# Optimization experiments

Hardware: AMD Instinct MI355X
Metric: run time of the kernel (lower is better)

## Reference

```python
import jax, jax.numpy as jnp
import numpy as np

K = 2  # top-k experts per token


def setup_inputs() -> dict:
    key = jax.random.key(0)
    k1, k2 = jax.random.split(key)
    B, T, D, E = 4, 4096, 4096, 64
    x = jax.random.normal(k1, (B, T, D), dtype=jnp.float32)
    W = jax.random.normal(k2, (E, D), dtype=jnp.float32) * (1.0 / np.sqrt(D))
    return {"x": x, "W": W}


def reference(x, W):
    # router_logits: [B, T, E]  (nn.Linear with no bias: x @ W.T)
    router_logits = jnp.einsum('btd,ed->bte', x, W)
    # top-k over expert dim, then softmax over the k selected logits
    topk_logits, topk_idx = jax.lax.top_k(router_logits, K)  # [B,T,K]
    topk_weight = jax.nn.softmax(topk_logits, axis=-1)       # [B,T,K]
    return (topk_idx, topk_weight, router_logits)
```

## Files before the change

### kernel.cpp

```cpp
#include <hip/hip_runtime.h>
#include <math.h>

#define NTOK 16384
#define DDIM 4096
#define NEXP 64
#define TAU  2e-4f
#define WS_LO 262144
#define NCW  16

typedef short bf16x8 __attribute__((ext_vector_type(8)));
typedef float f32x4  __attribute__((ext_vector_type(4)));

__device__ __forceinline__ unsigned short bf16_rne(float f) {
  unsigned u = __float_as_uint(f);
  u += 0x7fffu + ((u >> 16) & 1u);
  return (unsigned short)(u >> 16);
}

__device__ __forceinline__ void split4(float4 v, uint2& hi, uint2& lo) {
  unsigned h0 = bf16_rne(v.x), h1 = bf16_rne(v.y), h2 = bf16_rne(v.z), h3 = bf16_rne(v.w);
  float r0 = v.x - __uint_as_float(h0 << 16);
  float r1 = v.y - __uint_as_float(h1 << 16);
  float r2 = v.z - __uint_as_float(h2 << 16);
  float r3 = v.w - __uint_as_float(h3 << 16);
  unsigned l0 = bf16_rne(r0), l1 = bf16_rne(r1), l2 = bf16_rne(r2), l3 = bf16_rne(r3);
  hi = make_uint2(h0 | (h1 << 16), h2 | (h3 << 16));
  lo = make_uint2(l0 | (l1 << 16), l2 | (l3 << 16));
}

__device__ __forceinline__ void split4v(f32x4 v, uint2& hi, uint2& lo) {
  unsigned h0 = bf16_rne(v[0]), h1 = bf16_rne(v[1]), h2 = bf16_rne(v[2]), h3 = bf16_rne(v[3]);
  float r0 = v[0] - __uint_as_float(h0 << 16);
  float r1 = v[1] - __uint_as_float(h1 << 16);
  float r2 = v[2] - __uint_as_float(h2 << 16);
  float r3 = v[3] - __uint_as_float(h3 << 16);
  unsigned l0 = bf16_rne(r0), l1 = bf16_rne(r1), l2 = bf16_rne(r2), l3 = bf16_rne(r3);
  hi = make_uint2(h0 | (h1 << 16), h2 | (h3 << 16));
  lo = make_uint2(l0 | (l1 << 16), l2 | (l3 << 16));
}

__device__ __forceinline__ bf16x8 mk8(uint2 a, uint2 b) {
  union { uint4 u; bf16x8 v; } t;
  t.u = make_uint4(a.x, a.y, b.x, b.y);
  return t.v;
}

__device__ __forceinline__ void gld_lds16(const float* g, char* l) {
  __builtin_amdgcn_global_load_lds((const __attribute__((address_space(1))) void*)g,
                                   (__attribute__((address_space(3))) void*)l,
                                   16, 0, 0);
}

__device__ __forceinline__ bool better(float va, int ia, float vb, int ib) {
  return (va > vb) || (va == vb && ia < ib);
}
__device__ __forceinline__ bool betterd(double va, int ia, double vb, int ib) {
  return (va > vb) || (va == vb && ia < ib);
}
#define CE(va, ia, vb, ib) { if (better(vb, ib, va, ia)) { float _tv = va; va = vb; vb = _tv; int _ti = ia; ia = ib; ib = _ti; } }

__global__ __launch_bounds__(256)
void presplit_w(const float* __restrict__ w, short* __restrict__ ws) {
  const int tid = blockIdx.x * 256 + threadIdx.x;
  const int e = tid >> 9;
  const int o = tid & 511;
  const int c = o >> 2, q = o & 3;
  const int l = (e & 15) + 16 * q;
  const int g = e >> 4;
  const float* src = w + (size_t)e * DDIM + o * 8;
  float4 v0 = *(const float4*)src;
  float4 v1 = *(const float4*)(src + 4);
  uint2 h0, s0, h1, s1;
  split4(v0, h0, s0);
  split4(v1, h1, s1);
  const int off = c * 2048 + g * 512 + l * 8;
  *(uint4*)(ws + off)         = make_uint4(h0.x, h0.y, h1.x, h1.y);
  *(uint4*)(ws + WS_LO + off) = make_uint4(s0.x, s0.y, s1.x, s1.y);
}

__device__ __noinline__ void fixup_token(const float* __restrict__ x,
                                         const float* __restrict__ wgt,
                                         float* __restrict__ out_idx,
                                         float* __restrict__ out_wt,
                                         int tok, unsigned pk, int l) {
  const int e0 = pk & 255, e1 = (pk >> 8) & 255, e2 = (pk >> 16) & 255, e3 = (pk >> 24) & 255;
  const float* xr = x   + (size_t)tok * DDIM + l * 64;
  const float* w0 = wgt + (size_t)e0 * DDIM + l * 64;
  const float* w1 = wgt + (size_t)e1 * DDIM + l * 64;
  const float* w2 = wgt + (size_t)e2 * DDIM + l * 64;
  const float* w3 = wgt + (size_t)e3 * DDIM + l * 64;
  double s0 = 0.0, s1 = 0.0, s2 = 0.0, s3 = 0.0;
#pragma unroll 4
  for (int j = 0; j < 64; j += 4) {
    float4 xv = *(const float4*)(xr + j);
    float4 av = *(const float4*)(w0 + j);
    s0 = fma((double)xv.x, (double)av.x, s0); s0 = fma((double)xv.y, (double)av.y, s0);
    s0 = fma((double)xv.z, (double)av.z, s0); s0 = fma((double)xv.w, (double)av.w, s0);
    av = *(const float4*)(w1 + j);
    s1 = fma((double)xv.x, (double)av.x, s1); s1 = fma((double)xv.y, (double)av.y, s1);
    s1 = fma((double)xv.z, (double)av.z, s1); s1 = fma((double)xv.w, (double)av.w, s1);
    av = *(const float4*)(w2 + j);
    s2 = fma((double)xv.x, (double)av.x, s2); s2 = fma((double)xv.y, (double)av.y, s2);
    s2 = fma((double)xv.z, (double)av.z, s2); s2 = fma((double)xv.w, (double)av.w, s2);
    av = *(const float4*)(w3 + j);
    s3 = fma((double)xv.x, (double)av.x, s3); s3 = fma((double)xv.y, (double)av.y, s3);
    s3 = fma((double)xv.z, (double)av.z, s3); s3 = fma((double)xv.w, (double)av.w, s3);
  }
#pragma unroll
  for (int m = 1; m < 64; m <<= 1) {
    s0 += __shfl_xor(s0, m);
    s1 += __shfl_xor(s1, m);
    s2 += __shfl_xor(s2, m);
    s3 += __shfl_xor(s3, m);
  }
  if (l == 0) {
    double v0 = s0, v1 = s1, v2 = s2, v3 = s3;
    int i0 = e0, i1 = e1, i2 = e2, i3 = e3;
    if (betterd(v1, i1, v0, i0)) { double tv = v0; v0 = v1; v1 = tv; int ti = i0; i0 = i1; i1 = ti; }
    if (betterd(v3, i3, v2, i2)) { double tv = v2; v2 = v3; v3 = tv; int ti = i2; i2 = i3; i3 = ti; }
    if (betterd(v2, i2, v0, i0)) { double tv = v0; v0 = v2; v2 = tv; int ti = i0; i0 = i2; i2 = ti; }
    if (betterd(v3, i3, v1, i1)) { double tv = v1; v1 = v3; v3 = tv; int ti = i1; i1 = i3; i3 = ti; }
    if (betterd(v2, i2, v1, i1)) { double tv = v1; v1 = v2; v2 = tv; int ti = i1; i1 = i2; i2 = ti; }
    double ex = exp(v1 - v0);
    double den = 1.0 + ex;
    out_idx[tok * 2 + 0] = (float)i0;
    out_idx[tok * 2 + 1] = (float)i1;
    out_wt[tok * 2 + 0]  = (float)(1.0 / den);
    out_wt[tok * 2 + 1]  = (float)(ex / den);
  }
}

__global__ __launch_bounds__(512, 3)
void router_main(const float* __restrict__ x, const float* __restrict__ wgt,
                 const short* __restrict__ ws, float* __restrict__ out) {
  __shared__ __align__(16) char ldsbuf[65536];

  const int u = threadIdx.x;
  const int l = u & 63;
  const int wid = u >> 6;
  const int tokBase = blockIdx.x * 32;

  char* ring = ldsbuf + wid * 8192;
  const unsigned ldsbase =
      (unsigned)(size_t)(__attribute__((address_space(3))) char*)&ldsbuf[0];
  const unsigned rbase = ldsbase + wid * 8192 + l * 16;

  const int P = (blockIdx.x * 5) & 15;
#define PHYS(T) (((T) + P) & 15)

  const float* xA0 = x + (size_t)(tokBase +  0 + (l & 15)) * DDIM + wid * 512 + (l >> 4) * 8;
  const float* xB0 = xA0 + 4;
  const float* xA1 = x + (size_t)(tokBase + 16 + (l & 15)) * DDIM + wid * 512 + (l >> 4) * 8;
  const float* xB1 = xA1 + 4;

  const short* wch = ws + wid * 32768 + l * 8;

  f32x4 acc[2][4];
#pragma unroll
  for (int t2 = 0; t2 < 2; ++t2)
#pragma unroll
    for (int g = 0; g < 4; ++g) acc[t2][g] = (f32x4){0.f, 0.f, 0.f, 0.f};

  bf16x8 wset[2][8];

#define LDW(SET, T)                                                            \
  { const int cw_ = ((T) < NCW) ? (T) : NCW - 1;                               \
    const int cc_ = PHYS(cw_);                                                 \
    asm volatile("" ::: "memory");                                             \
    wset[SET][0] = *(const bf16x8*)(wch + cc_ * 2048 + 0 * 512);               \
    wset[SET][1] = *(const bf16x8*)(wch + WS_LO + cc_ * 2048 + 0 * 512);       \
    wset[SET][2] = *(const bf16x8*)(wch + cc_ * 2048 + 1 * 512);               \
    wset[SET][3] = *(const bf16x8*)(wch + WS_LO + cc_ * 2048 + 1 * 512);       \
    wset[SET][4] = *(const bf16x8*)(wch + cc_ * 2048 + 2 * 512);               \
    wset[SET][5] = *(const bf16x8*)(wch + WS_LO + cc_ * 2048 + 2 * 512);       \
    wset[SET][6] = *(const bf16x8*)(wch + cc_ * 2048 + 3 * 512);               \
    wset[SET][7] = *(const bf16x8*)(wch + WS_LO + cc_ * 2048 + 3 * 512);       \
    asm volatile("" ::: "memory"); }

#define XISSUE(T, SLOT)                                                        \
  { const int cx_ = ((T) < NCW) ? (T) : NCW - 1;                               \
    const int cp_ = PHYS(cx_) * 32;                                            \
    char* d_ = ring + (SLOT) * 4096;                                           \
    gld_lds16(xA0 + cp_, d_);                                                  \
    gld_lds16(xB0 + cp_, d_ + 1024);                                           \
    gld_lds16(xA1 + cp_, d_ + 2048);                                           \
    gld_lds16(xB1 + cp_, d_ + 3072); }

#define MM(T2, G, SET)                                                         \
  acc[T2][G] = __builtin_amdgcn_mfma_f32_16x16x32_bf16(ahi, wset[SET][2*(G)],   acc[T2][G], 0, 0, 0); \
  acc[T2][G] = __builtin_amdgcn_mfma_f32_16x16x32_bf16(ahi, wset[SET][2*(G)+1], acc[T2][G], 0, 0, 0); \
  acc[T2][G] = __builtin_amdgcn_mfma_f32_16x16x32_bf16(alo, wset[SET][2*(G)],   acc[T2][G], 0, 0, 0);

#define COMPT(T2, SET, F0, F1)                                                 \
  { uint2 h0_, s0_, h1_, s1_;                                                  \
    split4v(F0, h0_, s0_); split4v(F1, h1_, s1_);                              \
    bf16x8 ahi = mk8(h0_, h1_), alo = mk8(s0_, s1_);                           \
    MM(T2, 0, SET) MM(T2, 1, SET) MM(T2, 2, SET) MM(T2, 3, SET) }

#define STEP(T, SLOT, SET)                                                     \
  {                                                                            \
    asm volatile("s_waitcnt vmcnt(12)" ::: "memory");                          \
    f32x4 f0, f1, f2, f3;                                                      \
    { unsigned a_ = rbase + (SLOT) * 4096;                                     \
      asm volatile("ds_read_b128 %0, %2\n\tds_read_b128 %1, %2 offset:1024"    \
                   : "=&v"(f0), "=&v"(f1) : "v"(a_));                          \
      asm volatile("ds_read_b128 %0, %2 offset:2048\n\tds_read_b128 %1, %2 offset:3072" \
                   : "=&v"(f2), "=&v"(f3) : "v"(a_)); }                        \
    asm volatile("s_waitcnt lgkmcnt(0)" ::: "memory");                         \
    __builtin_amdgcn_sched_barrier(0);                                         \
    XISSUE((T) + 2, SLOT)                                                      \
    asm volatile("" ::: "memory");                                             \
    COMPT(0, SET, f0, f1)                                                      \
    COMPT(1, SET, f2, f3)                                                      \
    LDW(SET, (T) + 2)                                                          \
  }

  XISSUE(0, 0)
  LDW(0, 0)
  XISSUE(1, 1)
  LDW(1, 1)

  for (int t = 0; t < NCW; t += 2) {
    STEP(t, 0, 0)
    STEP(t + 1, 1, 1)
  }

  __syncthreads();
  float* p = (float*)ldsbuf;
#define PIDX(KQ, T2, G, R) ((((((KQ) * 2 + (T2)) * 4 + (G)) * 4 + (R)) << 6) + l)
#pragma unroll
  for (int t2 = 0; t2 < 2; ++t2)
#pragma unroll
    for (int g = 0; g < 4; ++g)
#pragma unroll
      for (int r = 0; r < 4; ++r)
        p[PIDX(wid, t2, g, r)] = acc[t2][g][r];
  __syncthreads();

  float* out_idx = out;
  float* out_wt  = out + NTOK * 2;
  float* out_lg  = out + NTOK * 4;

  {
    const int t2 = wid >> 2;
    const int r  = wid & 3;
    float v0 = 0.f, v1 = 0.f, v2 = 0.f, v3 = 0.f;
#pragma unroll
    for (int kq = 0; kq < 8; ++kq) {
      v0 += p[PIDX(kq, t2, 0, r)];
      v1 += p[PIDX(kq, t2, 1, r)];
      v2 += p[PIDX(kq, t2, 2, r)];
      v3 += p[PIDX(kq, t2, 3, r)];
    }

    const int tok = tokBase + t2 * 16 + (l >> 4) * 4 + r;
    {
      float* dst = out_lg + (size_t)tok * NEXP + (l & 15);
      dst[0]  = v0;
      dst[16] = v1;
      dst[32] = v2;
      dst[48] = v3;
    }

    const int cbase = (l & 15);
    int i0 = cbase, i1 = cbase + 16, i2 = cbase + 32, i3 = cbase + 48;
    CE(v0, i0, v1, i1) CE(v2, i2, v3, i3) CE(v0, i0, v2, i2) CE(v1, i1, v3, i3) CE(v1, i1, v2, i2)
#pragma unroll
    for (int m = 1; m <= 8; m <<= 1) {
      float p0 = __shfl_xor(v0, m), p1 = __shfl_xor(v1, m);
      float p2 = __shfl_xor(v2, m), p3 = __shfl_xor(v3, m);
      int j0 = __shfl_xor(i0, m), j1 = __shfl_xor(i1, m);
      int j2 = __shfl_xor(i2, m), j3 = __shfl_xor(i3, m);
      CE(v0, i0, p3, j3) CE(v1, i1, p2, j2) CE(v2, i2, p1, j1) CE(v3, i3, p0, j0)
      CE(v0, i0, v2, i2) CE(v1, i1, v3, i3) CE(v0, i0, v1, i1) CE(v2, i2, v3, i3)
    }

    bool flag = false;
    unsigned pk = 0;
    if (cbase == 0) {
      flag = (v0 - v1 < TAU) || (v1 - v2 < TAU) || (v2 - v3 < TAU);
      pk = (unsigned)i0 | ((unsigned)i1 << 8) | ((unsigned)i2 << 16) | ((unsigned)i3 << 24);
      if (!flag) {
        float ex = expf(v1 - v0);
        float den = 1.0f + ex;
        out_idx[tok * 2 + 0] = (float)i0;
        out_idx[tok * 2 + 1] = (float)i1;
        out_wt[tok * 2 + 0]  = 1.0f / den;
        out_wt[tok * 2 + 1]  = ex / den;
      }
    }
    unsigned long long mk = __ballot(flag);
    while (mk) {
      const int src = __builtin_ctzll(mk);
      mk &= mk - 1;
      const unsigned pks = (unsigned)__shfl((int)pk, src);
      fixup_token(x, wgt, out_idx, out_wt, tokBase + t2 * 16 + (src >> 4) * 4 + r, pks, l);
    }
  }
}

extern "C" void kernel_launch(void* const* d_in, const int* in_sizes, int n_in,
                              void* d_out, int out_size, void* d_ws, size_t ws_size,
                              hipStream_t stream) {
  const float* x = (const float*)d_in[0];
  const float* w = (const float*)d_in[1];
  float* out = (float*)d_out;
  short* ws = (short*)d_ws;

  hipLaunchKernelGGL(presplit_w, dim3(128), dim3(256), 0, stream, w, ws);
  hipLaunchKernelGGL(router_main, dim3(NTOK / 32), dim3(512), 0, stream, x, w, ws, out);
}
```

Before: 91.49 us.

## Halve weight register buffering, split weight loads mid-MFMA, raise occupancy to four

```diff
diff --git a/kernel.cpp b/kernel.cpp
--- a/kernel.cpp
+++ b/kernel.cpp
@@ -130,7 +130,7 @@
   }
 }
 
-__global__ __launch_bounds__(512, 3)
+__global__ __launch_bounds__(512, 4)
 void router_main(const float* __restrict__ x, const float* __restrict__ wgt,
                  const short* __restrict__ ws, float* __restrict__ out) {
   __shared__ __align__(16) char ldsbuf[65536];
@@ -149,9 +149,7 @@
 #define PHYS(T) (((T) + P) & 15)
 
   const float* xA0 = x + (size_t)(tokBase +  0 + (l & 15)) * DDIM + wid * 512 + (l >> 4) * 8;
-  const float* xB0 = xA0 + 4;
   const float* xA1 = x + (size_t)(tokBase + 16 + (l & 15)) * DDIM + wid * 512 + (l >> 4) * 8;
-  const float* xB1 = xA1 + 4;
 
   const short* wch = ws + wid * 32768 + l * 8;
 
@@ -161,20 +159,26 @@
 #pragma unroll
     for (int g = 0; g < 4; ++g) acc[t2][g] = (f32x4){0.f, 0.f, 0.f, 0.f};
 
-  bf16x8 wset[2][8];
-
-#define LDW(SET, T)                                                            \
+  bf16x8 wset[8];
+
+#define LDW_A(T)                                                               \
   { const int cw_ = ((T) < NCW) ? (T) : NCW - 1;                               \
     const int cc_ = PHYS(cw_);                                                 \
     asm volatile("" ::: "memory");                                             \
-    wset[SET][0] = *(const bf16x8*)(wch + cc_ * 2048 + 0 * 512);               \
-    wset[SET][1] = *(const bf16x8*)(wch + WS_LO + cc_ * 2048 + 0 * 512);       \
-    wset[SET][2] = *(const bf16x8*)(wch + cc_ * 2048 + 1 * 512);               \
-    wset[SET][3] = *(const bf16x8*)(wch + WS_LO + cc_ * 2048 + 1 * 512);       \
-    wset[SET][4] = *(const bf16x8*)(wch + cc_ * 2048 + 2 * 512);               \
-    wset[SET][5] = *(const bf16x8*)(wch + WS_LO + cc_ * 2048 + 2 * 512);       \
-    wset[SET][6] = *(const bf16x8*)(wch + cc_ * 2048 + 3 * 512);               \
-    wset[SET][7] = *(const bf16x8*)(wch + WS_LO + cc_ * 2048 + 3 * 512);       \
+    wset[0] = *(const bf16x8*)(wch + cc_ * 2048 + 0 * 512);                    \
+    wset[1] = *(const bf16x8*)(wch + WS_LO + cc_ * 2048 + 0 * 512);            \
+    wset[2] = *(const bf16x8*)(wch + cc_ * 2048 + 1 * 512);                    \
+    wset[3] = *(const bf16x8*)(wch + WS_LO + cc_ * 2048 + 1 * 512);            \
+    asm volatile("" ::: "memory"); }
+
+#define LDW_B(T)                                                               \
+  { const int cw_ = ((T) < NCW) ? (T) : NCW - 1;                               \
+    const int cc_ = PHYS(cw_);                                                 \
+    asm volatile("" ::: "memory");                                             \
+    wset[4] = *(const bf16x8*)(wch + cc_ * 2048 + 2 * 512);                    \
+    wset[5] = *(const bf16x8*)(wch + WS_LO + cc_ * 2048 + 2 * 512);            \
+    wset[6] = *(const bf16x8*)(wch + cc_ * 2048 + 3 * 512);                    \
+    wset[7] = *(const bf16x8*)(wch + WS_LO + cc_ * 2048 + 3 * 512);            \
     asm volatile("" ::: "memory"); }
 
 #define XISSUE(T, SLOT)                                                        \
@@ -182,47 +186,47 @@
     const int cp_ = PHYS(cx_) * 32;                                            \
     char* d_ = ring + (SLOT) * 4096;                                           \
     gld_lds16(xA0 + cp_, d_);                                                  \
-    gld_lds16(xB0 + cp_, d_ + 1024);                                           \
+    gld_lds16(xA0 + cp_ + 4, d_ + 1024);                                       \
     gld_lds16(xA1 + cp_, d_ + 2048);                                           \
-    gld_lds16(xB1 + cp_, d_ + 3072); }
-
-#define MM(T2, G, SET)                                                         \
-  acc[T2][G] = __builtin_amdgcn_mfma_f32_16x16x32_bf16(ahi, wset[SET][2*(G)],   acc[T2][G], 0, 0, 0); \
-  acc[T2][G] = __builtin_amdgcn_mfma_f32_16x16x32_bf16(ahi, wset[SET][2*(G)+1], acc[T2][G], 0, 0, 0); \
-  acc[T2][G] = __builtin_amdgcn_mfma_f32_16x16x32_bf16(alo, wset[SET][2*(G)],   acc[T2][G], 0, 0, 0);
-
-#define COMPT(T2, SET, F0, F1)                                                 \
-  { uint2 h0_, s0_, h1_, s1_;                                                  \
-    split4v(F0, h0_, s0_); split4v(F1, h1_, s1_);                              \
-    bf16x8 ahi = mk8(h0_, h1_), alo = mk8(s0_, s1_);                           \
-    MM(T2, 0, SET) MM(T2, 1, SET) MM(T2, 2, SET) MM(T2, 3, SET) }
-
-#define STEP(T, SLOT, SET)                                                     \
+    gld_lds16(xA1 + cp_ + 4, d_ + 3072); }
+
+#define MM(T2, G, AHI, ALO)                                                    \
+  acc[T2][G] = __builtin_amdgcn_mfma_f32_16x16x32_bf16(AHI, wset[2*(G)],   acc[T2][G], 0, 0, 0); \
+  acc[T2][G] = __builtin_amdgcn_mfma_f32_16x16x32_bf16(AHI, wset[2*(G)+1], acc[T2][G], 0, 0, 0); \
+  acc[T2][G] = __builtin_amdgcn_mfma_f32_16x16x32_bf16(ALO, wset[2*(G)],   acc[T2][G], 0, 0, 0);
+
+#define STEP(T)                                                                \
   {                                                                            \
-    asm volatile("s_waitcnt vmcnt(12)" ::: "memory");                          \
+    asm volatile("s_waitcnt vmcnt(4)" ::: "memory");                           \
     f32x4 f0, f1, f2, f3;                                                      \
-    { unsigned a_ = rbase + (SLOT) * 4096;                                     \
+    { unsigned a_ = rbase + ((T) & 1) * 4096;                                  \
       asm volatile("ds_read_b128 %0, %2\n\tds_read_b128 %1, %2 offset:1024"    \
                    : "=&v"(f0), "=&v"(f1) : "v"(a_));                          \
       asm volatile("ds_read_b128 %0, %2 offset:2048\n\tds_read_b128 %1, %2 offset:3072" \
                    : "=&v"(f2), "=&v"(f3) : "v"(a_)); }                        \
     asm volatile("s_waitcnt lgkmcnt(0)" ::: "memory");                         \
     __builtin_amdgcn_sched_barrier(0);                                         \
-    XISSUE((T) + 2, SLOT)                                                      \
-    asm volatile("" ::: "memory");                                             \
-    COMPT(0, SET, f0, f1)                                                      \
-    COMPT(1, SET, f2, f3)                                                      \
-    LDW(SET, (T) + 2)                                                          \
+    uint2 h0_, s0_, h1_, s1_;                                                  \
+    split4v(f0, h0_, s0_); split4v(f1, h1_, s1_);                              \
+    bf16x8 a0hi = mk8(h0_, h1_), a0lo = mk8(s0_, s1_);                         \
+    split4v(f2, h0_, s0_); split4v(f3, h1_, s1_);                              \
+    bf16x8 a1hi = mk8(h0_, h1_), a1lo = mk8(s0_, s1_);                         \
+    MM(0, 0, a0hi, a0lo) MM(0, 1, a0hi, a0lo)                                  \
+    MM(1, 0, a1hi, a1lo) MM(1, 1, a1hi, a1lo)                                  \
+    LDW_A((T) + 1)                                                             \
+    MM(0, 2, a0hi, a0lo) MM(0, 3, a0hi, a0lo)                                  \
+    MM(1, 2, a1hi, a1lo) MM(1, 3, a1hi, a1lo)                                  \
+    LDW_B((T) + 1)                                                             \
+    XISSUE((T) + 2, (T) & 1)                                                   \
   }
 
   XISSUE(0, 0)
-  LDW(0, 0)
+  LDW_A(0) LDW_B(0)
   XISSUE(1, 1)
-  LDW(1, 1)
-
-  for (int t = 0; t < NCW; t += 2) {
-    STEP(t, 0, 0)
-    STEP(t + 1, 1, 1)
+
+#pragma unroll
+  for (int t = 0; t < NCW; ++t) {
+    STEP(t)
   }
 
   __syncthreads();
```

Result: faster. 85.22 us (-6.9%).
